# Optimization experiments

Hardware: AMD Instinct MI355X
Metric: run time of the kernel (lower is better)

Reference implementation:

```python
import jax, jax.numpy as jnp
import numpy as np
from jax import lax

B, S, D, H, L = 16, 1024, 768, 512, 128


def _ln(x, g, b, eps=1e-5):
    m = jnp.mean(x, -1, keepdims=True)
    v = jnp.mean((x - m) ** 2, -1, keepdims=True)
    return (x - m) / jnp.sqrt(v + eps) * g + b


def setup_inputs() -> dict:
    key = jax.random.key(0)
    ks = iter(jax.random.split(key, 64))
    def w(*shape):
        return jax.random.normal(next(ks), shape, jnp.float32) * 0.02
    def z(*shape):
        return jnp.zeros(shape, jnp.float32)
    def o(*shape):
        return jnp.ones(shape, jnp.float32)
    return dict(
        sequences=jax.random.normal(next(ks), (B, S, D), jnp.float32),
        W1=w(D, H), b1=z(H), g1=o(H), be1=z(H),
        Wv=w(H, H), bv=z(H), Wo=w(H, H), bo=z(H),
        W2=w(H, H), b2=z(H), g2=o(H), be2=z(H),
        W3=w(H, L), b3=z(L), g3=o(L), be3=z(L),
        W4=w(L, H), b4=z(H), g4=o(H), be4=z(H),
        W5=w(H, L), b5=z(L), g5=o(L), be5=z(L),
        Wd1=w(L, H), bd1=z(H), gd1=o(H), bed1=z(H),
        Wd2=w(H, H), bd2=z(H), gd2=o(H), bed2=z(H),
        Wd3=w(H, D), bd3=z(D),
        Wm=w(D, D), Um=w(D, D), bm=z(D),
    )


def reference(sequences, W1, b1, g1, be1, Wv, bv, Wo, bo, W2, b2, g2, be2,
              W3, b3, g3, be3, W4, b4, g4, be4, W5, b5, g5, be5,
              Wd1, bd1, gd1, bed1, Wd2, bd2, gd2, bed2, Wd3, bd3,
              Wm, Um, bm):
    x = sequences
    rw, tw, cw, xw, l2w = 1.0, 0.3, 0.3, 0.1, 1e-4  # loss weights from __init__

    def encode(t):
        h = jax.nn.relu(_ln(t @ W1 + b1, g1, be1))       # encoder_local (dropout=eval)
        a = (h @ Wv + bv) @ Wo + bo                       # seq-len-1 self-attn == out_proj(v_proj(h))
        g = jax.nn.relu(_ln(a @ W2 + b2, g2, be2))        # encoder_global
        zl = _ln(g @ W3 + b3, g3, be3)
        e = jax.nn.relu(_ln(zl @ W4 + b4, g4, be4))       # emotion_projector
        return _ln(e @ W5 + b5, g5, be5)

    def decode(zl):
        h = jax.nn.relu(_ln(zl @ Wd1 + bd1, gd1, bed1))   # decoder_global
        h = jax.nn.relu(_ln(h @ Wd2 + bd2, gd2, bed2))    # decoder_local
        return h @ Wd3 + bd3

    # memory_system recurrence: mem_j = tanh(x_j Wm + mem_{j-1} Um + bm)
    def step(mem, xt):
        new = jnp.tanh(xt @ Wm + mem @ Um + bm)
        return new, new
    _, mems = lax.scan(step, jnp.zeros((x.shape[0], x.shape[2]), x.dtype),
                       jnp.swapaxes(x, 0, 1))
    mem = jnp.swapaxes(mems, 0, 1)  # [B,S,D]

    lat = encode(x)          # [B,S,L] latent of current token
    lat_mem = encode(mem)    # [B,S,L] latent of memory context
    z0 = encode(jnp.zeros((x.shape[2],), x.dtype))  # latent of zero bert_context at j=0
    lat_prev = jnp.concatenate(
        [jnp.broadcast_to(z0, (x.shape[0], 1, z0.shape[-1])), lat[:, :-1]], axis=1)

    recon = jnp.clip(jnp.mean((decode(lat) - x) ** 2, -1), 0.0, 10.0)
    trans = jnp.clip(jnp.mean((lat - lat_prev) ** 2, -1), 0.0, 10.0)
    eps = 1e-8
    nl = lat / jnp.maximum(jnp.linalg.norm(lat, axis=-1, keepdims=True), eps)
    nm = lat_mem / jnp.maximum(jnp.linalg.norm(lat_mem, axis=-1, keepdims=True), eps)
    ctx = jnp.clip(1.0 - jnp.sum(nl * nm, -1), 0.0, 10.0)
    contrastive = 0.0  # 1x1 cross-entropy over a single logit is identically zero

    params = [W1, b1, g1, be1, Wv, bv, Wo, bo, W2, b2, g2, be2, W3, b3, g3, be3,
              W4, b4, g4, be4, W5, b5, g5, be5, Wd1, bd1, gd1, bed1,
              Wd2, bd2, gd2, bed2, Wd3, bd3, Wm, Um, bm]
    l2 = jnp.clip(sum(jnp.linalg.norm(p) for p in params), 0.0, 10.0)

    per_tok = jnp.clip(rw * recon + tw * trans + cw * ctx + xw * contrastive + l2w * l2,
                       0.0, 100.0)  # [B,S]
    return jnp.sum(per_tok) / x.shape[0]
```

## Files before the change

### kernel.cpp

```cpp
#include <hip/hip_runtime.h>

#define DI __device__ __forceinline__

typedef __attribute__((ext_vector_type(8))) short short8v;
typedef __attribute__((ext_vector_type(4))) float f32x4;

DI short f2bf(float f) {
  unsigned u = __float_as_uint(f);
  u += 0x7fffu + ((u >> 16) & 1u);
  return (short)(u >> 16);
}

DI float waveRed(float v) {
#pragma unroll
  for (int m = 32; m; m >>= 1) v += __shfl_xor(v, m, 64);
  return v;
}

DI float tanh_fast(float x) {
  float ax = fabsf(x);
  float e = __expf(2.f * ax);
  float t = 1.f - 2.f / (e + 1.f);
  return copysignf(t, x);
}

DI void gl16(const void* g, void* l) {
  __builtin_amdgcn_global_load_lds((const __attribute__((address_space(1))) void*)g,
                                   (__attribute__((address_space(3))) void*)l, 16, 0, 0);
}

template <int BF16OUT>
__global__ __launch_bounds__(256) void gemm_k(const short* __restrict__ A,
                                              const short* __restrict__ BT,
                                              const float* __restrict__ bias,
                                              void* __restrict__ C, int M, int N, int K) {
  __shared__ short sA[2][8][512];
  __shared__ short sB[2][8][512];
  const int tid = threadIdx.x, lane = tid & 63, wid = tid >> 6;
  const int tm = blockIdx.x << 7, tn = blockIdx.y << 7;
  const int wm = wid >> 1, wn = wid & 1;
  const int r15 = lane & 15, kq = (lane >> 4) << 3;
  const int KT = K >> 5;

  f32x4 acc[4][4];
#pragma unroll
  for (int i = 0; i < 4; i++)
#pragma unroll
    for (int j = 0; j < 4; j++) acc[i][j] = f32x4{0.f, 0.f, 0.f, 0.f};

  auto stage = [&](int kt, int buf) {
    const int k0 = kt << 5;
#pragma unroll
    for (int i = 0; i < 2; i++) {
      const int st = (wid << 1) | i;
      gl16(A + (size_t)(tm + (st << 4) + r15) * K + k0 + kq, &sA[buf][st][0]);
      gl16(BT + (size_t)(tn + (st << 4) + r15) * K + k0 + kq, &sB[buf][st][0]);
    }
  };

  stage(0, 0);
  __syncthreads();
  int cur = 0;
  for (int kt = 0; kt < KT; ++kt) {
    if (kt + 1 < KT) stage(kt + 1, cur ^ 1);
    short8v a[4], b[4];
#pragma unroll
    for (int i = 0; i < 4; i++) a[i] = *(const short8v*)&sA[cur][(wm << 2) | i][lane << 3];
#pragma unroll
    for (int j = 0; j < 4; j++) b[j] = *(const short8v*)&sB[cur][(wn << 2) | j][lane << 3];
#pragma unroll
    for (int i = 0; i < 4; i++)
#pragma unroll
      for (int j = 0; j < 4; j++)
        acc[i][j] = __builtin_amdgcn_mfma_f32_16x16x32_bf16(a[i], b[j], acc[i][j], 0, 0, 0);
    __syncthreads();
    cur ^= 1;
  }

#pragma unroll
  for (int j = 0; j < 4; j++) {
    const int col = tn + (wn << 6) + (j << 4) + r15;
    const float bs = bias[col];
#pragma unroll
    for (int i = 0; i < 4; i++) {
      const int row0 = tm + (wm << 6) + (i << 4) + ((lane >> 4) << 2);
#pragma unroll
      for (int rr = 0; rr < 4; rr++) {
        const float v = acc[i][j][rr] + bs;
        const size_t off = (size_t)(row0 + rr) * N + col;
        if (BF16OUT)
          ((short*)C)[off] = f2bf(v);
        else
          ((float*)C)[off] = v;
      }
    }
  }
}

template <int RELU, int WF32>
__global__ __launch_bounds__(256) void ln_k(const float* __restrict__ in,
                                            const float* __restrict__ ga,
                                            const float* __restrict__ be,
                                            short* __restrict__ ob, float* __restrict__ of,
                                            int N) {
  const int row = blockIdx.x;
  const float* r = in + (size_t)row * N;
  float s = 0.f, s2 = 0.f;
  for (int c = threadIdx.x; c < N; c += 256) {
    float v = r[c];
    s += v;
    s2 += v * v;
  }
  s = waveRed(s);
  s2 = waveRed(s2);
  __shared__ float ps[4], ps2[4];
  const int w = threadIdx.x >> 6;
  if ((threadIdx.x & 63) == 0) { ps[w] = s; ps2[w] = s2; }
  __syncthreads();
  if (threadIdx.x == 0) {
    float a = 0.f, b = 0.f;
    for (int i = 0; i < 4; i++) { a += ps[i]; b += ps2[i]; }
    ps[0] = a; ps2[0] = b;
  }
  __syncthreads();
  const float mean = ps[0] / N;
  float var = ps2[0] / N - mean * mean;
  var = fmaxf(var, 0.f);
  const float rstd = rsqrtf(var + 1e-5f);
  for (int c = threadIdx.x; c < N; c += 256) {
    float v = (r[c] - mean) * rstd * ga[c] + be[c];
    if (RELU) v = fmaxf(v, 0.f);
    ob[(size_t)row * N + c] = f2bf(v);
    if (WF32) of[(size_t)row * N + c] = v;
  }
}

struct TT { const float* src; short* dst; int K; int N; };
struct TTab { TT t[12]; int pref[13]; };

__global__ __launch_bounds__(256) void tr_k(TTab tab) {
  const int bid = blockIdx.x;
  int seg = 0;
  while (seg < 11 && bid >= tab.pref[seg + 1]) ++seg;
  const int lt = bid - tab.pref[seg];
  const int K = tab.t[seg].K, N = tab.t[seg].N;
  const int tncnt = N >> 5;
  const int tk = lt / tncnt, tn = lt % tncnt;
  __shared__ float tile[32][33];
  const int x = threadIdx.x & 31, y = threadIdx.x >> 5;
  const float* src = tab.t[seg].src;
  short* dst = tab.t[seg].dst;
#pragma unroll
  for (int i = 0; i < 4; i++) {
    const int kk = (tk << 5) + y + (i << 3);
    tile[y + (i << 3)][x] = src[(size_t)kk * N + (tn << 5) + x];
  }
  __syncthreads();
#pragma unroll
  for (int i = 0; i < 4; i++) {
    const int nn = (tn << 5) + y + (i << 3);
    dst[(size_t)nn * K + (tk << 5) + x] = f2bf(tile[x][y + (i << 3)]);
  }
}

__global__ __launch_bounds__(256) void cvt_k(const float* __restrict__ in,
                                             short* __restrict__ outp, int n4) {
  const int i = blockIdx.x * 256 + threadIdx.x;
  if (i < n4) {
    float4 v = ((const float4*)in)[i];
    short4 o;
    o.x = f2bf(v.x); o.y = f2bf(v.y); o.z = f2bf(v.z); o.w = f2bf(v.w);
    ((short4*)outp)[i] = o;
  }
}

__global__ __launch_bounds__(128) void recur_k(const short* __restrict__ UmT,
                                               const float* __restrict__ xWm,
                                               short* __restrict__ mems, short* ping,
                                               unsigned int* flags) {
  __shared__ short um[144 * 512];
  __shared__ float red[6 * 256];
  const int tid = threadIdx.x, lane = tid & 63, wv = tid >> 6, wg = blockIdx.x;
  const int n0 = wg * 96;

  for (int f = wv; f < 144; f += 2) {
    const int nt = f / 24, kf = f % 24;
    const int col = n0 + nt * 16 + (lane & 15);
    const int kk = kf * 32 + ((lane >> 4) << 3);
    *(short8v*)(um + ((size_t)f * 64 + lane) * 8) =
        *(const short8v*)(UmT + (size_t)col * 768 + kk);
  }
  __syncthreads();

  for (int t = 0; t < 1024; ++t) {
    const short* mi = ping + (t & 1) * (16 * 768);
    short* mo = ping + ((t & 1) ^ 1) * (16 * 768);

    float xw[3][4];
#pragma unroll
    for (int j = 0; j < 3; j++) {
      const int nt = wv * 3 + j;
      const int col = n0 + nt * 16 + (lane & 15);
#pragma unroll
      for (int rr = 0; rr < 4; rr++) {
        const int b = ((lane >> 4) << 2) + rr;
        xw[j][rr] = xWm[((size_t)b * 1024 + t) * 768 + col];
      }
    }

    if (t) {
      if (tid < 8) {
        while (__hip_atomic_load(&flags[tid * 32], __ATOMIC_ACQUIRE,
                                 __HIP_MEMORY_SCOPE_AGENT) < (unsigned)t)
          __builtin_amdgcn_s_sleep(2);
      }
      __syncthreads();
    }

    short8v Af[12];
#pragma unroll
    for (int i = 0; i < 12; i++) {
      const int kk = (wv * 12 + i) * 32 + ((lane >> 4) << 3);
      Af[i] = *(const short8v*)(mi + (size_t)(lane & 15) * 768 + kk);
    }

    f32x4 acc[6];
#pragma unroll
    for (int n = 0; n < 6; n++) acc[n] = f32x4{0.f, 0.f, 0.f, 0.f};
#pragma unroll
    for (int i = 0; i < 12; i++) {
      const int kf = wv * 12 + i;
#pragma unroll
      for (int n = 0; n < 6; n++) {
        short8v b = *(const short8v*)(um + (((size_t)n * 24 + kf) * 64 + lane) * 8);
        acc[n] = __builtin_amdgcn_mfma_f32_16x16x32_bf16(Af[i], b, acc[n], 0, 0, 0);
      }
    }

#define RW(NT)                                                                   \
  {                                                                              \
    _Pragma("unroll") for (int rr = 0; rr < 4; rr++)                             \
        red[(NT)*256 + (lane << 2) + rr] = acc[NT][rr];                          \
  }
    if (wv == 0) { RW(3) RW(4) RW(5) } else { RW(0) RW(1) RW(2) }
    __syncthreads();

#define EPI(J, NT)                                                               \
  {                                                                              \
    const int col = n0 + (NT)*16 + (lane & 15);                                  \
    _Pragma("unroll") for (int rr = 0; rr < 4; rr++) {                           \
      const int b = ((lane >> 4) << 2) + rr;                                     \
      float v = acc[NT][rr] + red[(NT)*256 + (lane << 2) + rr] + xw[J][rr];      \
      v = tanh_fast(v);                                                          \
      const short bf = f2bf(v);                                                  \
      mo[(size_t)b * 768 + col] = bf;                                            \
      mems[((size_t)b * 1024 + t) * 768 + col] = bf;                             \
    }                                                                            \
  }
    if (wv == 0) { EPI(0, 0) EPI(1, 1) EPI(2, 2) } else { EPI(0, 3) EPI(1, 4) EPI(2, 5) }

    __threadfence();
    __syncthreads();
    if (tid == 0)
      __hip_atomic_store(&flags[wg * 32], (unsigned)(t + 1), __ATOMIC_RELEASE,
                         __HIP_MEMORY_SCOPE_AGENT);
  }
#undef RW
#undef EPI
}

struct PTab { const float* p[37]; int pref[38]; };

__global__ __launch_bounds__(128) void ssq_k(PTab tab, float* ssq) {
  const int bid = blockIdx.x;
  int seg = 0;
  while (seg < 36 && bid >= tab.pref[seg + 1]) ++seg;
  const int off = (bid - tab.pref[seg]) * 128 + threadIdx.x;
  float v = tab.p[seg][off];
  v = waveRed(v * v);
  __shared__ float pp[2];
  if ((threadIdx.x & 63) == 0) pp[threadIdx.x >> 6] = v;
  __syncthreads();
  if (threadIdx.x == 0) atomicAdd(&ssq[seg], pp[0] + pp[1]);
}

__global__ void l2_k(const float* ssq, float* l2) {
  float s = 0.f;
  for (int i = 0; i < 37; i++) s += sqrtf(ssq[i]);
  l2[0] = fminf(fmaxf(s, 0.f), 10.f);
}

__global__ __launch_bounds__(256) void loss_k(const float* __restrict__ x,
                                              const float* __restrict__ dec,
                                              const float* __restrict__ lat,
                                              const float* __restrict__ l2p,
                                              float* __restrict__ out) {
  const int r = blockIdx.x;
  const int s = r & 1023;
  const float* dr = dec + (size_t)r * 768;
  const float* xr = x + (size_t)r * 768;
  float rs = 0.f;
  for (int c = threadIdx.x; c < 768; c += 256) {
    const float d = dr[c] - xr[c];
    rs += d * d;
  }
  const float* L = lat + (size_t)r * 128;
  const float* Lm = lat + (size_t)(16384 + r) * 128;
  const float* Lp = s ? (L - 128) : (lat + (size_t)32768 * 128);
  float ts = 0.f, dp = 0.f, nl = 0.f, nm = 0.f;
  for (int c = threadIdx.x; c < 128; c += 256) {
    const float a = L[c], m = Lm[c], p = Lp[c];
    const float d = a - p;
    ts += d * d; dp += a * m; nl += a * a; nm += m * m;
  }
  rs = waveRed(rs); ts = waveRed(ts); dp = waveRed(dp); nl = waveRed(nl); nm = waveRed(nm);
  __shared__ float pr[5][4];
  const int w = threadIdx.x >> 6;
  if ((threadIdx.x & 63) == 0) { pr[0][w] = rs; pr[1][w] = ts; pr[2][w] = dp; pr[3][w] = nl; pr[4][w] = nm; }
  __syncthreads();
  if (threadIdx.x == 0) {
    float R = 0, T = 0, Dp = 0, NL = 0, NM = 0;
    for (int i = 0; i < 4; i++) { R += pr[0][i]; T += pr[1][i]; Dp += pr[2][i]; NL += pr[3][i]; NM += pr[4][i]; }
    const float recon = fminf(fmaxf(R / 768.f, 0.f), 10.f);
    const float trans = fminf(fmaxf(T / 128.f, 0.f), 10.f);
    float ctx = 1.f - Dp / (fmaxf(sqrtf(NL), 1e-8f) * fmaxf(sqrtf(NM), 1e-8f));
    ctx = fminf(fmaxf(ctx, 0.f), 10.f);
    float pt = recon + 0.3f * trans + 0.3f * ctx + 1e-4f * l2p[0];
    pt = fminf(fmaxf(pt, 0.f), 100.f);
    atomicAdd(out, pt * 0.0625f);
  }
}

extern "C" void kernel_launch(void* const* d_in, const int* in_sizes, int n_in, void* d_out,
                              int out_size, void* d_ws, size_t ws_size, hipStream_t stream) {
  const float* X = (const float*)d_in[0];
  const float* W1 = (const float*)d_in[1];
  const float* b1 = (const float*)d_in[2];
  const float* g1 = (const float*)d_in[3];
  const float* be1 = (const float*)d_in[4];
  const float* Wv = (const float*)d_in[5];
  const float* bv = (const float*)d_in[6];
  const float* Wo = (const float*)d_in[7];
  const float* bo = (const float*)d_in[8];
  const float* W2 = (const float*)d_in[9];
  const float* b2 = (const float*)d_in[10];
  const float* g2 = (const float*)d_in[11];
  const float* be2 = (const float*)d_in[12];
  const float* W3 = (const float*)d_in[13];
  const float* b3 = (const float*)d_in[14];
  const float* g3 = (const float*)d_in[15];
  const float* be3 = (const float*)d_in[16];
  const float* W4 = (const float*)d_in[17];
  const float* b4 = (const float*)d_in[18];
  const float* g4 = (const float*)d_in[19];
  const float* be4 = (const float*)d_in[20];
  const float* W5 = (const float*)d_in[21];
  const float* b5 = (const float*)d_in[22];
  const float* g5 = (const float*)d_in[23];
  const float* be5 = (const float*)d_in[24];
  const float* Wd1 = (const float*)d_in[25];
  const float* bd1 = (const float*)d_in[26];
  const float* gd1 = (const float*)d_in[27];
  const float* bed1 = (const float*)d_in[28];
  const float* Wd2 = (const float*)d_in[29];
  const float* bd2 = (const float*)d_in[30];
  const float* gd2 = (const float*)d_in[31];
  const float* bed2 = (const float*)d_in[32];
  const float* Wd3 = (const float*)d_in[33];
  const float* bd3 = (const float*)d_in[34];
  const float* Wm = (const float*)d_in[35];
  const float* Um = (const float*)d_in[36];
  const float* bm = (const float*)d_in[37];

  char* ws = (char*)d_ws;
  size_t off = 0;
  auto alloc = [&](size_t bytes) -> char* {
    char* p = ws + off;
    off += (bytes + 255) & ~(size_t)255;
    return p;
  };
  const int ME = 32896;

  float* SH = (float*)alloc((size_t)ME * 512 * 4);
  short* A0 = (short*)alloc((size_t)ME * 768 * 2);
  short* B1 = (short*)alloc((size_t)ME * 512 * 2);
  short* B2 = (short*)alloc((size_t)ME * 512 * 2);
  float* LATf = (float*)alloc((size_t)ME * 128 * 4);
  short* W1T = (short*)alloc(512 * 768 * 2);
  short* WvT = (short*)alloc(512 * 512 * 2);
  short* WoT = (short*)alloc(512 * 512 * 2);
  short* W2T = (short*)alloc(512 * 512 * 2);
  short* W3T = (short*)alloc(128 * 512 * 2);
  short* W4T = (short*)alloc(512 * 128 * 2);
  short* W5T = (short*)alloc(128 * 512 * 2);
  short* Wd1T = (short*)alloc(512 * 128 * 2);
  short* Wd2T = (short*)alloc(512 * 512 * 2);
  short* Wd3T = (short*)alloc(768 * 512 * 2);
  short* WmT = (short*)alloc(768 * 768 * 2);
  short* UmT = (short*)alloc(768 * 768 * 2);
  char* MISC = alloc(49152 + 1024 + 512);
  short* PING = (short*)MISC;
  unsigned int* FLAGS = (unsigned int*)(MISC + 49152);
  float* SSQ = (float*)(MISC + 49152 + 1024);
  float* L2V = (float*)(MISC + 49152 + 1024 + 256);

  float* XWM = SH;
  float* F1 = SH;
  float* F2 = SH;
  float* DEC = SH;
  short* Z1 = B1;
  short* LATb = B1;
  (void)ws_size; (void)n_in; (void)out_size;

  hipMemsetAsync(A0 + (size_t)32768 * 768, 0, (size_t)128 * 768 * 2, stream);
  hipMemsetAsync(MISC, 0, 49152 + 1024 + 512, stream);
  hipMemsetAsync(d_out, 0, sizeof(float), stream);

  TTab tt;
  int acc = 0;
  auto addT = [&](int i, const float* s, short* d, int K, int N) {
    tt.t[i] = TT{s, d, K, N};
    tt.pref[i] = acc;
    acc += (K / 32) * (N / 32);
  };
  addT(0, W1, W1T, 768, 512);
  addT(1, Wv, WvT, 512, 512);
  addT(2, Wo, WoT, 512, 512);
  addT(3, W2, W2T, 512, 512);
  addT(4, W3, W3T, 512, 128);
  addT(5, W4, W4T, 128, 512);
  addT(6, W5, W5T, 512, 128);
  addT(7, Wd1, Wd1T, 128, 512);
  addT(8, Wd2, Wd2T, 512, 512);
  addT(9, Wd3, Wd3T, 512, 768);
  addT(10, Wm, WmT, 768, 768);
  addT(11, Um, UmT, 768, 768);
  tt.pref[12] = acc;
  tr_k<<<acc, 256, 0, stream>>>(tt);

  cvt_k<<<(16384 * 768 / 4 + 255) / 256, 256, 0, stream>>>(X, A0, 16384 * 768 / 4);

  gemm_k<0><<<dim3(16384 / 128, 6), 256, 0, stream>>>(A0, WmT, bm, XWM, 16384, 768, 768);

  recur_k<<<8, 128, 0, stream>>>(UmT, XWM, A0 + (size_t)16384 * 768, PING, FLAGS);

  gemm_k<0><<<dim3(ME / 128, 4), 256, 0, stream>>>(A0, W1T, b1, F1, ME, 512, 768);
  ln_k<1, 0><<<ME, 256, 0, stream>>>(F1, g1, be1, B1, nullptr, 512);
  gemm_k<1><<<dim3(ME / 128, 4), 256, 0, stream>>>(B1, WvT, bv, B2, ME, 512, 512);
  gemm_k<1><<<dim3(ME / 128, 4), 256, 0, stream>>>(B2, WoT, bo, B1, ME, 512, 512);
  gemm_k<0><<<dim3(ME / 128, 4), 256, 0, stream>>>(B1, W2T, b2, F1, ME, 512, 512);
  ln_k<1, 0><<<ME, 256, 0, stream>>>(F1, g2, be2, B2, nullptr, 512);
  gemm_k<0><<<dim3(ME / 128, 1), 256, 0, stream>>>(B2, W3T, b3, F2, ME, 128, 512);
  ln_k<0, 0><<<ME, 256, 0, stream>>>(F2, g3, be3, Z1, nullptr, 128);
  gemm_k<0><<<dim3(ME / 128, 4), 256, 0, stream>>>(Z1, W4T, b4, F1, ME, 512, 128);
  ln_k<1, 0><<<ME, 256, 0, stream>>>(F1, g4, be4, B1, nullptr, 512);
  gemm_k<0><<<dim3(ME / 128, 1), 256, 0, stream>>>(B1, W5T, b5, F2, ME, 128, 512);
  ln_k<0, 1><<<ME, 256, 0, stream>>>(F2, g5, be5, LATb, LATf, 128);

  gemm_k<0><<<dim3(16384 / 128, 4), 256, 0, stream>>>(LATb, Wd1T, bd1, F1, 16384, 512, 128);
  ln_k<1, 0><<<16384, 256, 0, stream>>>(F1, gd1, bed1, B2, nullptr, 512);
  gemm_k<0><<<dim3(16384 / 128, 4), 256, 0, stream>>>(B2, Wd2T, bd2, F1, 16384, 512, 512);
  ln_k<1, 0><<<16384, 256, 0, stream>>>(F1, gd2, bed2, B1, nullptr, 512);
  gemm_k<0><<<dim3(16384 / 128, 6), 256, 0, stream>>>(B1, Wd3T, bd3, DEC, 16384, 768, 512);

  PTab pt;
  int blk = 0;
  for (int i = 0; i < 37; i++) {
    pt.p[i] = (const float*)d_in[i + 1];
    pt.pref[i] = blk;
    blk += in_sizes[i + 1] / 128;
  }
  pt.pref[37] = blk;
  ssq_k<<<blk, 128, 0, stream>>>(pt, SSQ);
  l2_k<<<1, 1, 0, stream>>>(SSQ, L2V);

  loss_k<<<16384, 256, 0, stream>>>(X, DEC, LATf, L2V, (float*)d_out);
}
```

Before: 6.795 ms.

## Replace flag-based grid sync in recurrence with tagged 64-bit data packets

The sequential memory recurrence kernel no longer uses per-workgroup flags with a threadfence, a release store and an acquire spin followed by a block barrier. Each 64-bit word now packs three bf16 hidden values plus a 16-bit timestep tag. Consumers spin directly on the data words until every tag matches, which removes a fence and a round trip of flag latency from each of the 1024 serial steps. In exchange each element costs more bytes, the A operand needs packing and unpacking through shared staging, and correctness rests on relaxed 64-bit atomics being single-copy atomic.

Result: no change. 6.855 ms (+0.9%).

```diff
diff --git a/kernel.cpp b/kernel.cpp
--- a/kernel.cpp
+++ b/kernel.cpp
@@ -4,6 +4,7 @@
 
 typedef __attribute__((ext_vector_type(8))) short short8v;
 typedef __attribute__((ext_vector_type(4))) float f32x4;
+typedef unsigned long long u64;
 
 DI short f2bf(float f) {
   unsigned u = __float_as_uint(f);
@@ -176,10 +177,11 @@
 
 __global__ __launch_bounds__(128) void recur_k(const short* __restrict__ UmT,
                                                const float* __restrict__ xWm,
-                                               short* __restrict__ mems, short* ping,
-                                               unsigned int* flags) {
+                                               short* __restrict__ mems,
+                                               u64* __restrict__ ping) {
   __shared__ short um[144 * 512];
   __shared__ float red[6 * 256];
+  __shared__ short stg[2][16][52];
   const int tid = threadIdx.x, lane = tid & 63, wv = tid >> 6, wg = blockIdx.x;
   const int n0 = wg * 96;
 
@@ -192,9 +194,14 @@
   }
   __syncthreads();
 
+  const int crow = lane & 15;
+  const size_t cbase = (size_t)crow * 288 + (size_t)(wv * 48 + (lane >> 4)) * 3;
+  const int prow = lane >> 2, l4 = lane & 3;
+  const size_t pbase = (size_t)prow * 288 + (size_t)(wg * 36 + wv * 18);
+
   for (int t = 0; t < 1024; ++t) {
-    const short* mi = ping + (t & 1) * (16 * 768);
-    short* mo = ping + ((t & 1) ^ 1) * (16 * 768);
+    const u64* mi = ping + (size_t)(t & 1) * (16 * 288);
+    u64* mo = ping + (size_t)((t & 1) ^ 1) * (16 * 288);
 
     float xw[3][4];
 #pragma unroll
@@ -208,32 +215,39 @@
       }
     }
 
-    if (t) {
-      if (tid < 8) {
-        while (__hip_atomic_load(&flags[tid * 32], __ATOMIC_ACQUIRE,
-                                 __HIP_MEMORY_SCOPE_AGENT) < (unsigned)t)
-          __builtin_amdgcn_s_sleep(2);
+    u64 q[12][3];
+    const unsigned tg = (unsigned)t;
+    while (true) {
+#pragma unroll
+      for (int i = 0; i < 12; i++) {
+        const u64* p = mi + cbase + i * 12;
+        q[i][0] = __hip_atomic_load(p, __ATOMIC_RELAXED, __HIP_MEMORY_SCOPE_AGENT);
+        q[i][1] = __hip_atomic_load(p + 1, __ATOMIC_RELAXED, __HIP_MEMORY_SCOPE_AGENT);
+        q[i][2] = __hip_atomic_load(p + 2, __ATOMIC_RELAXED, __HIP_MEMORY_SCOPE_AGENT);
       }
-      __syncthreads();
+      unsigned bad = 0;
+#pragma unroll
+      for (int i = 0; i < 12; i++)
+        bad |= (unsigned)((q[i][0] >> 48) ^ tg) | (unsigned)((q[i][1] >> 48) ^ tg) |
+               (unsigned)((q[i][2] >> 48) ^ tg);
+      if (__all(bad == 0)) break;
     }
 
-    short8v Af[12];
+    f32x4 acc[6];
+#pragma unroll
+    for (int n = 0; n < 6; n++) acc[n] = f32x4{0.f, 0.f, 0.f, 0.f};
 #pragma unroll
     for (int i = 0; i < 12; i++) {
-      const int kk = (wv * 12 + i) * 32 + ((lane >> 4) << 3);
-      Af[i] = *(const short8v*)(mi + (size_t)(lane & 15) * 768 + kk);
-    }
-
-    f32x4 acc[6];
-#pragma unroll
-    for (int n = 0; n < 6; n++) acc[n] = f32x4{0.f, 0.f, 0.f, 0.f};
-#pragma unroll
-    for (int i = 0; i < 12; i++) {
+      union { unsigned u[4]; short8v s; } A;
+      A.u[0] = (unsigned)(q[i][0] & 0xFFFFFFFFull);
+      A.u[1] = (unsigned)((q[i][0] >> 32) & 0xFFFFull) | ((unsigned)(q[i][1] & 0xFFFFull) << 16);
+      A.u[2] = (unsigned)((q[i][1] >> 16) & 0xFFFFFFFFull);
+      A.u[3] = (unsigned)(q[i][2] & 0xFFFFFFFFull);
       const int kf = wv * 12 + i;
 #pragma unroll
       for (int n = 0; n < 6; n++) {
         short8v b = *(const short8v*)(um + (((size_t)n * 24 + kf) * 64 + lane) * 8);
-        acc[n] = __builtin_amdgcn_mfma_f32_16x16x32_bf16(Af[i], b, acc[n], 0, 0, 0);
+        acc[n] = __builtin_amdgcn_mfma_f32_16x16x32_bf16(A.s, b, acc[n], 0, 0, 0);
       }
     }
 
@@ -253,17 +267,33 @@
       float v = acc[NT][rr] + red[(NT)*256 + (lane << 2) + rr] + xw[J][rr];      \
       v = tanh_fast(v);                                                          \
       const short bf = f2bf(v);                                                  \
-      mo[(size_t)b * 768 + col] = bf;                                            \
       mems[((size_t)b * 1024 + t) * 768 + col] = bf;                             \
+      stg[wv][b][(J)*16 + (lane & 15)] = bf;                                     \
     }                                                                            \
   }
     if (wv == 0) { EPI(0, 0) EPI(1, 1) EPI(2, 2) } else { EPI(0, 3) EPI(1, 4) EPI(2, 5) }
 
-    __threadfence();
-    __syncthreads();
-    if (tid == 0)
-      __hip_atomic_store(&flags[wg * 32], (unsigned)(t + 1), __ATOMIC_RELEASE,
-                         __HIP_MEMORY_SCOPE_AGENT);
+    asm volatile("s_waitcnt lgkmcnt(0)" ::: "memory");
+
+    const u64 tgs = (u64)(unsigned)(t + 1) << 48;
+#pragma unroll
+    for (int rep = 0; rep < 5; ++rep) {
+      const int w = l4 + rep * 4;
+      if (w < 18) {
+        const int c = (w * 11) >> 5;
+        const int p = w - 3 * c;
+        const int col = c * 8 + p * 3;
+        u64 s0 = (unsigned short)stg[wv][prow][col];
+        u64 s1 = (unsigned short)stg[wv][prow][col + 1];
+        u64 s2 = (unsigned short)stg[wv][prow][col + 2];
+        if (p == 2) s2 = 0;
+        const u64 qv = s0 | (s1 << 16) | (s2 << 32) | tgs;
+        __hip_atomic_store(mo + pbase + w, qv, __ATOMIC_RELAXED, __HIP_MEMORY_SCOPE_AGENT);
+      }
+    }
+
+    asm volatile("s_waitcnt lgkmcnt(0)" ::: "memory");
+    __builtin_amdgcn_s_barrier();
   }
 #undef RW
 #undef EPI
@@ -398,11 +428,10 @@
   short* Wd3T = (short*)alloc(768 * 512 * 2);
   short* WmT = (short*)alloc(768 * 768 * 2);
   short* UmT = (short*)alloc(768 * 768 * 2);
-  char* MISC = alloc(49152 + 1024 + 512);
-  short* PING = (short*)MISC;
-  unsigned int* FLAGS = (unsigned int*)(MISC + 49152);
-  float* SSQ = (float*)(MISC + 49152 + 1024);
-  float* L2V = (float*)(MISC + 49152 + 1024 + 256);
+  char* MISC = alloc(73728 + 512);
+  u64* PING = (u64*)MISC;
+  float* SSQ = (float*)(MISC + 73728);
+  float* L2V = (float*)(MISC + 73728 + 256);
 
   float* XWM = SH;
   float* F1 = SH;
@@ -413,7 +442,7 @@
   (void)ws_size; (void)n_in; (void)out_size;
 
   hipMemsetAsync(A0 + (size_t)32768 * 768, 0, (size_t)128 * 768 * 2, stream);
-  hipMemsetAsync(MISC, 0, 49152 + 1024 + 512, stream);
+  hipMemsetAsync(MISC, 0, 73728 + 512, stream);
   hipMemsetAsync(d_out, 0, sizeof(float), stream);
 
   TTab tt;
@@ -442,7 +471,7 @@
 
   gemm_k<0><<<dim3(16384 / 128, 6), 256, 0, stream>>>(A0, WmT, bm, XWM, 16384, 768, 768);
 
-  recur_k<<<8, 128, 0, stream>>>(UmT, XWM, A0 + (size_t)16384 * 768, PING, FLAGS);
+  recur_k<<<8, 128, 0, stream>>>(UmT, XWM, A0 + (size_t)16384 * 768, PING);
 
   gemm_k<0><<<dim3(ME / 128, 4), 256, 0, stream>>>(A0, W1T, b1, F1, ME, 512, 768);
   ln_k<1, 0><<<ME, 256, 0, stream>>>(F1, g1, be1, B1, nullptr, 512);
```
